# Kernel tuning notes

Measured on AMD Instinct MI355X. Metric: run time of the kernel, lower is better.

Reference implementation:

```python
import jax, jax.numpy as jnp
import numpy as np

N_NODES = 100000


def _gcn_conv(x, src, dst, dinv, W, b, n):
    # x: [n, din] -> [n, dout]; PyG GCNConv: transform, then normalized scatter-sum, then bias
    h = x @ W                                   # [n, dout]
    norm = dinv[src] * dinv[dst]                # [E'] symmetric normalization
    msg = h[src] * norm[:, None]                # gather + scale (irregular access)
    out = jax.ops.segment_sum(msg, dst, num_segments=n)
    return out + b


def _add_self_loops(edge_index, n):
    loop = jnp.arange(n, dtype=edge_index.dtype)
    src = jnp.concatenate([edge_index[0], loop])
    dst = jnp.concatenate([edge_index[1], loop])
    return src, dst


def setup_inputs() -> dict:
    key = jax.random.key(0)
    k1, k2, k3, k4 = jax.random.split(key, 4)
    n, e = N_NODES, 1000000
    din, dhid, dout = 512, 512, 128
    x = jax.random.normal(k1, (n, din), dtype=jnp.float32)
    edge_index = jax.random.randint(k2, (2, e), 0, n, dtype=jnp.int64)
    W1 = jax.random.normal(k3, (din, dhid), dtype=jnp.float32) * (1.0 / np.sqrt(din))
    b1 = jnp.zeros((dhid,), dtype=jnp.float32)
    W2 = jax.random.normal(k4, (dhid, dout), dtype=jnp.float32) * (1.0 / np.sqrt(dhid))
    b2 = jnp.zeros((dout,), dtype=jnp.float32)
    return {"x": x, "edge_index": edge_index, "original_size": n,
            "W1": W1, "b1": b1, "W2": W2, "b2": b2}


def reference(x, edge_index, original_size, W1, b1, W2, b2):
    n = x.shape[0]
    src, dst = _add_self_loops(edge_index, n)
    # degree over destination (with self-loops deg >= 1)
    deg = jnp.zeros((n,), dtype=x.dtype).at[dst].add(1.0)
    dinv = deg ** -0.5
    h = _gcn_conv(x, src, dst, dinv, W1, b1, n)
    out = _gcn_conv(h, src, dst, dinv, W2, b2, n)
    return out[:original_size]
```

## Files before the change

### kernel.cpp

```cpp
#include <hip/hip_runtime.h>
#include <hip/hip_bf16.h>


typedef __attribute__((ext_vector_type(8))) short short8;
typedef __attribute__((ext_vector_type(4))) float f32x4;

#define DIN 512
#define DOUT 128

__device__ inline short f2bs(float f) {
    __hip_bfloat16 h = __float2bfloat16(f);
    return __builtin_bit_cast(short, h);
}
__device__ inline float b2f(const void* p, long long idx) {
    return __bfloat162float(((const __hip_bfloat16*)p)[idx]);
}
__device__ inline int edge_at(const void* ei, int eflag, long long idx) {
    return eflag ? ((const int*)ei)[idx] : (int)((const long long*)ei)[idx];
}

__global__ void k_fdetect(const unsigned short* __restrict__ xr, int* __restrict__ fflag) {
    __shared__ int cnt;
    if (threadIdx.x == 0) cnt = 0;
    __syncthreads();
    int local = 0;
    for (int i = threadIdx.x; i < 8192; i += 256) {
        unsigned e = (xr[i] >> 7) & 0xFF;
        if (e == 0 || (e >= 0x70 && e <= 0x8E)) local++;
    }
    atomicAdd(&cnt, local);
    __syncthreads();
    if (threadIdx.x == 0) *fflag = (cnt >= 7373) ? 1 : 0;
}

__global__ void k_edetect(const int* __restrict__ ei_raw, int* __restrict__ eflag) {
    __shared__ int any;
    if (threadIdx.x == 0) any = 0;
    __syncthreads();
    for (int i = threadIdx.x; i < 4096; i += 256)
        if (ei_raw[2 * i + 1] != 0) any = 1;
    __syncthreads();
    if (threadIdx.x == 0) *eflag = any;
}

__global__ __launch_bounds__(256) void k_w12(const void* __restrict__ W1,
                                             const void* __restrict__ W2,
                                             const int* __restrict__ fflag,
                                             __hip_bfloat16* __restrict__ w12p) {
    int t = blockIdx.x * 256 + threadIdx.x;
    int d = t >> 7, j = t & 127;
    float acc = 0.f;
    if (*fflag) {
        for (int c = 0; c < 512; ++c)
            acc += b2f(W1, d * 512 + c) * b2f(W2, c * 128 + j);
    } else {
        const float* w1 = (const float*)W1;
        const float* w2 = (const float*)W2;
        for (int c = 0; c < 512; ++c)
            acc += w1[d * 512 + c] * w2[c * 128 + j];
    }
    int ks = d >> 5, r = d & 31;
    int quad = r >> 3, jj = r & 7;
    int nc = j >> 4, m16 = j & 15;
    w12p[(((size_t)(ks * 8 + nc) * 64) + quad * 16 + m16) * 8 + jj] = __float2bfloat16(acc);
}

__global__ void k_b12(const void* __restrict__ b1, const void* __restrict__ W2,
                      const int* __restrict__ fflag, float* __restrict__ b12) {
    int j = threadIdx.x;
    float acc = 0.f;
    if (*fflag) {
        for (int c = 0; c < 512; ++c)
            acc += b2f(b1, c) * b2f(W2, c * 128 + j);
    } else {
        const float* bb = (const float*)b1;
        const float* w2 = (const float*)W2;
        for (int c = 0; c < 512; ++c)
            acc += bb[c] * w2[c * 128 + j];
    }
    b12[j] = acc;
}

__global__ __launch_bounds__(256) void k_deg(const void* __restrict__ ei,
                                             const int* __restrict__ eflag, int E,
                                             int* __restrict__ degi) {
    int e = blockIdx.x * 256 + threadIdx.x;
    if (e >= E) return;
    atomicAdd(&degi[edge_at(ei, *eflag, (long long)E + e)], 1);
}

__global__ __launch_bounds__(256) void k_scan1(const int* __restrict__ degi,
                                               int* __restrict__ row_ptr,
                                               int* __restrict__ blocksum,
                                               float* __restrict__ dinv, int n) {
    __shared__ int sh[256];
    int t = threadIdx.x, g = blockIdx.x * 256 + t;
    int val = (g < n) ? degi[g] : 0;
    if (g < n) dinv[g] = rsqrtf((float)(val + 1));
    sh[t] = val;
    __syncthreads();
    for (int o = 1; o < 256; o <<= 1) {
        int v = (t >= o) ? sh[t - o] : 0;
        __syncthreads();
        if (t >= o) sh[t] += v;
        __syncthreads();
    }
    if (g < n) row_ptr[g] = sh[t] - val;
    if (t == 255) blocksum[blockIdx.x] = sh[255];
}

__global__ void k_scan2(int* __restrict__ blocksum, int nb) {
    __shared__ int sh[512];
    int t = threadIdx.x;
    int val = (t < nb) ? blocksum[t] : 0;
    sh[t] = val;
    __syncthreads();
    for (int o = 1; o < 512; o <<= 1) {
        int v = (t >= o) ? sh[t - o] : 0;
        __syncthreads();
        if (t >= o) sh[t] += v;
        __syncthreads();
    }
    if (t < nb) blocksum[t] = sh[t] - val;
}

__global__ __launch_bounds__(256) void k_scan3(int* __restrict__ row_ptr,
                                               int* __restrict__ cursor,
                                               const int* __restrict__ blocksum,
                                               int n, int E) {
    int g = blockIdx.x * 256 + threadIdx.x;
    if (g == 0) row_ptr[n] = E;
    if (g >= n) return;
    int v = row_ptr[g] + blocksum[blockIdx.x];
    row_ptr[g] = v;
    cursor[g] = v;
}

__global__ __launch_bounds__(256) void k_fill(const void* __restrict__ ei,
                                              const int* __restrict__ eflag, int E,
                                              const float* __restrict__ dinv,
                                              int* __restrict__ cursor,
                                              int2* __restrict__ csr) {
    int e = blockIdx.x * 256 + threadIdx.x;
    if (e >= E) return;
    int f = *eflag;
    int s = edge_at(ei, f, e);
    int d = edge_at(ei, f, (long long)E + e);
    int pos = atomicAdd(&cursor[d], 1);
    csr[pos] = make_int2(s, __float_as_int(dinv[s]));
}

__global__ __launch_bounds__(256) void k_gemm(const void* __restrict__ xv,
                                              const short* __restrict__ w12p,
                                              const int* __restrict__ fflag,
                                              float* __restrict__ M, int n) {
    int wave = (blockIdx.x * 256 + threadIdx.x) >> 6;
    int lane = threadIdx.x & 63;
    int row0 = wave * 16;
    if (row0 >= n) return;
    int quad = lane >> 4, m16 = lane & 15;
    const short8* Bp = (const short8*)w12p;

    f32x4 acc[8];
#pragma unroll
    for (int j = 0; j < 8; ++j) acc[j] = (f32x4){0.f, 0.f, 0.f, 0.f};

    int ra = row0 + m16;
    if (ra >= n) ra = n - 1;

    if (*fflag) {
        const short* xs = (const short*)xv;
#pragma unroll 4
        for (int ks = 0; ks < 16; ++ks) {
            int k0 = ks * 32 + quad * 8;
            short8 A0 = *(const short8*)(xs + (size_t)ra * 512 + k0);
#pragma unroll
            for (int nc = 0; nc < 8; ++nc) {
                short8 B = Bp[(ks * 8 + nc) * 64 + lane];
                acc[nc] = __builtin_amdgcn_mfma_f32_16x16x32_bf16(A0, B, acc[nc], 0, 0, 0);
            }
        }
    } else {
        const float* xf = (const float*)xv;
#pragma unroll 4
        for (int ks = 0; ks < 16; ++ks) {
            int k0 = ks * 32 + quad * 8;
            float4 u0 = *(const float4*)(xf + (size_t)ra * 512 + k0);
            float4 u1 = *(const float4*)(xf + (size_t)ra * 512 + k0 + 4);
            short8 A0;
            A0[0] = f2bs(u0.x); A0[1] = f2bs(u0.y); A0[2] = f2bs(u0.z); A0[3] = f2bs(u0.w);
            A0[4] = f2bs(u1.x); A0[5] = f2bs(u1.y); A0[6] = f2bs(u1.z); A0[7] = f2bs(u1.w);
#pragma unroll
            for (int nc = 0; nc < 8; ++nc) {
                short8 B = Bp[(ks * 8 + nc) * 64 + lane];
                acc[nc] = __builtin_amdgcn_mfma_f32_16x16x32_bf16(A0, B, acc[nc], 0, 0, 0);
            }
        }
    }
#pragma unroll
    for (int nc = 0; nc < 8; ++nc)
#pragma unroll
        for (int r = 0; r < 4; ++r) {
            int row = row0 + quad * 4 + r;
            if (row < n)
                M[(size_t)row * 128 + nc * 16 + m16] = acc[nc][r];
        }
}

template <bool FINAL>
__global__ __launch_bounds__(256) void k_gather(const int* __restrict__ row_ptr,
                                                const int2* __restrict__ csr,
                                                const float* __restrict__ dinv,
                                                const float* __restrict__ src_feat,
                                                float* __restrict__ dstf,
                                                const float* __restrict__ b12,
                                                const void* __restrict__ b2,
                                                const int* __restrict__ fflag,
                                                void* __restrict__ out, int n) {
    int d = blockIdx.x * 4 + (threadIdx.x >> 6);
    if (d >= n) return;
    int lane = threadIdx.x & 63;
    int half = lane >> 5, sl = lane & 31;
    int c = sl * 4;
    float di = dinv[d];
    float ax = 0.f, ay = 0.f, az = 0.f, aw = 0.f, wsum = 0.f;
    if (half == 0) {
        float4 s = *(const float4*)(src_feat + (size_t)d * 128 + c);
        ax = di * s.x; ay = di * s.y; az = di * s.z; aw = di * s.w;
    }
    int beg = row_ptr[d], end = row_ptr[d + 1];
    for (int e = beg + half; e < end; e += 2) {
        int2 rec = csr[e];
        float w = __int_as_float(rec.y);
        float4 v = *(const float4*)(src_feat + (size_t)rec.x * 128 + c);
        ax += w * v.x; ay += w * v.y; az += w * v.z; aw += w * v.w;
        wsum += w;
    }
    ax += __shfl_xor(ax, 32);
    ay += __shfl_xor(ay, 32);
    az += __shfl_xor(az, 32);
    aw += __shfl_xor(aw, 32);
    wsum += __shfl_xor(wsum, 32);
    if (half) return;
    ax *= di; ay *= di; az *= di; aw *= di;
    if (!FINAL) {
        *(float4*)(dstf + (size_t)d * 128 + c) = make_float4(ax, ay, az, aw);
    } else {
        float coef = di * (wsum + di);
        float o0 = ax + coef * b12[c];
        float o1 = ay + coef * b12[c + 1];
        float o2 = az + coef * b12[c + 2];
        float o3 = aw + coef * b12[c + 3];
        if (*fflag) {
            o0 += b2f(b2, c);     o1 += b2f(b2, c + 1);
            o2 += b2f(b2, c + 2); o3 += b2f(b2, c + 3);
            ushort4 u = make_ushort4((unsigned short)f2bs(o0), (unsigned short)f2bs(o1),
                                     (unsigned short)f2bs(o2), (unsigned short)f2bs(o3));
            *(ushort4*)((unsigned short*)out + (size_t)d * 128 + c) = u;
        } else {
            o0 += ((const float*)b2)[c];
            o1 += ((const float*)b2)[c + 1];
            o2 += ((const float*)b2)[c + 2];
            o3 += ((const float*)b2)[c + 3];
            *(float4*)((float*)out + (size_t)d * 128 + c) = make_float4(o0, o1, o2, o3);
        }
    }
}

__global__ __launch_bounds__(256) void k_sentinel(unsigned short* __restrict__ out, int total) {
    int t = blockIdx.x * 256 + threadIdx.x;
    if (t < total) out[t] = 0x4641;
}

extern "C" void kernel_launch(void* const* d_in, const int* in_sizes, int n_in,
                              void* d_out, int out_size, void* d_ws, size_t ws_size,
                              hipStream_t stream) {
    const int n = out_size / DOUT;

    const void *x = nullptr, *W1 = nullptr, *b1 = nullptr, *W2 = nullptr, *b2 = nullptr;
    const void* ei_raw = nullptr;
    int E = 0;
    const long long nx = (long long)n * DIN;
    for (int i = 0; i < n_in; ++i) {
        long long s = in_sizes[i];
        if      (s == nx && !x)                      x  = d_in[i];
        else if (s == (long long)DIN * DIN && !W1)   W1 = d_in[i];
        else if (s == (long long)DIN && !b1)         b1 = d_in[i];
        else if (s == (long long)DIN * DOUT && !W2)  W2 = d_in[i];
        else if (s == (long long)DOUT && !b2)        b2 = d_in[i];
        else if (s == 1) {  }
        else if (!ei_raw) { ei_raw = d_in[i]; E = (int)(s / 2); }
    }
    if (!x || !W1 || !b1 || !W2 || !b2 || !ei_raw) {
        x  = d_in[0];
        ei_raw = d_in[1];  E = in_sizes[1] / 2;
        W1 = d_in[3]; b1 = d_in[4]; W2 = d_in[5]; b2 = d_in[6];
    }

    const int nb_scan = (n + 255) / 256;

    char* ws = (char*)d_ws;
    size_t off = 0;
    auto alloc = [&](size_t bytes) { void* p = ws + off; off = (off + bytes + 255) & ~255ULL; return p; };
    int*   eflag    = (int*)alloc(4);
    int*   fflag    = (int*)alloc(4);
    int*   degi     = (int*)alloc((size_t)n * 4);
    float* dinv     = (float*)alloc((size_t)n * 4);
    float* b12      = (float*)alloc(DOUT * 4);
    __hip_bfloat16* w12p = (__hip_bfloat16*)alloc(DIN * DOUT * 2);
    int*   row_ptr  = (int*)alloc(((size_t)n + 1) * 4);
    int*   cursor   = (int*)alloc((size_t)n * 4);
    int*   blocksum = (int*)alloc(512 * 4);
    int2*  csr      = (int2*)alloc((size_t)E * 8);
    float* M        = (float*)alloc((size_t)n * DOUT * 4);
    float* B1       = (float*)alloc((size_t)n * DOUT * 4);

    if (ws_size < off) {
        k_sentinel<<<(out_size + 255) / 256, 256, 0, stream>>>((unsigned short*)d_out, out_size);
        return;
    }

    hipMemsetAsync(degi, 0, (size_t)n * 4, stream);

    k_fdetect<<<1, 256, 0, stream>>>((const unsigned short*)x, fflag);
    k_edetect<<<1, 256, 0, stream>>>((const int*)ei_raw, eflag);

    k_w12<<<(DIN * DOUT) / 256, 256, 0, stream>>>(W1, W2, fflag, w12p);
    k_b12<<<1, 128, 0, stream>>>(b1, W2, fflag, b12);

    k_deg<<<(E + 255) / 256, 256, 0, stream>>>(ei_raw, eflag, E, degi);
    k_scan1<<<nb_scan, 256, 0, stream>>>(degi, row_ptr, blocksum, dinv, n);
    k_scan2<<<1, 512, 0, stream>>>(blocksum, nb_scan);
    k_scan3<<<nb_scan, 256, 0, stream>>>(row_ptr, cursor, blocksum, n, E);
    k_fill<<<(E + 255) / 256, 256, 0, stream>>>(ei_raw, eflag, E, dinv, cursor, csr);

    int waves = (n + 15) / 16;
    k_gemm<<<(waves + 3) / 4, 256, 0, stream>>>(x, (const short*)w12p, fflag, M, n);

    int nb_g = (n + 3) / 4;
    k_gather<false><<<nb_g, 256, 0, stream>>>(row_ptr, csr, dinv, M, B1,
                                              nullptr, nullptr, fflag, nullptr, n);
    k_gather<true><<<nb_g, 256, 0, stream>>>(row_ptr, csr, dinv, B1, nullptr,
                                             b12, b2, fflag, d_out, n);
}
```

Before: 697.2 us.

## Vectorize W12 precompute, tile GEMM over 64 rows, batch gather rows per wave

```diff
diff --git a/kernel.cpp b/kernel.cpp
--- a/kernel.cpp
+++ b/kernel.cpp
@@ -14,6 +14,9 @@
 }
 __device__ inline float b2f(const void* p, long long idx) {
     return __bfloat162float(((const __hip_bfloat16*)p)[idx]);
+}
+__device__ inline float bsu(unsigned short v) {
+    return __bfloat162float(__builtin_bit_cast(__hip_bfloat16, v));
 }
 __device__ inline int edge_at(const void* ei, int eflag, long long idx) {
     return eflag ? ((const int*)ei)[idx] : (int)((const long long*)ei)[idx];
@@ -48,21 +51,44 @@
                                              const int* __restrict__ fflag,
                                              __hip_bfloat16* __restrict__ w12p) {
     int t = blockIdx.x * 256 + threadIdx.x;
-    int d = t >> 7, j = t & 127;
-    float acc = 0.f;
+    int d = t >> 5, j0 = (t & 31) * 4;
+    float4 acc = make_float4(0.f, 0.f, 0.f, 0.f);
     if (*fflag) {
-        for (int c = 0; c < 512; ++c)
-            acc += b2f(W1, d * 512 + c) * b2f(W2, c * 128 + j);
+        const short* w1s = (const short*)W1;
+        const unsigned short* w2u = (const unsigned short*)W2;
+        for (int c8 = 0; c8 < 512; c8 += 8) {
+            short8 av = *(const short8*)(w1s + (size_t)d * 512 + c8);
+#pragma unroll
+            for (int k = 0; k < 8; ++k) {
+                float a = bsu((unsigned short)av[k]);
+                ushort4 u = *(const ushort4*)(w2u + (size_t)(c8 + k) * 128 + j0);
+                acc.x += a * bsu(u.x); acc.y += a * bsu(u.y);
+                acc.z += a * bsu(u.z); acc.w += a * bsu(u.w);
+            }
+        }
     } else {
         const float* w1 = (const float*)W1;
         const float* w2 = (const float*)W2;
-        for (int c = 0; c < 512; ++c)
-            acc += w1[d * 512 + c] * w2[c * 128 + j];
+        for (int c4 = 0; c4 < 512; c4 += 4) {
+            float4 a  = *(const float4*)(w1 + (size_t)d * 512 + c4);
+            float4 r0 = *(const float4*)(w2 + (size_t)(c4 + 0) * 128 + j0);
+            float4 r1 = *(const float4*)(w2 + (size_t)(c4 + 1) * 128 + j0);
+            float4 r2 = *(const float4*)(w2 + (size_t)(c4 + 2) * 128 + j0);
+            float4 r3 = *(const float4*)(w2 + (size_t)(c4 + 3) * 128 + j0);
+            acc.x += a.x * r0.x + a.y * r1.x + a.z * r2.x + a.w * r3.x;
+            acc.y += a.x * r0.y + a.y * r1.y + a.z * r2.y + a.w * r3.y;
+            acc.z += a.x * r0.z + a.y * r1.z + a.z * r2.z + a.w * r3.z;
+            acc.w += a.x * r0.w + a.y * r1.w + a.z * r2.w + a.w * r3.w;
+        }
     }
     int ks = d >> 5, r = d & 31;
     int quad = r >> 3, jj = r & 7;
-    int nc = j >> 4, m16 = j & 15;
-    w12p[(((size_t)(ks * 8 + nc) * 64) + quad * 16 + m16) * 8 + jj] = __float2bfloat16(acc);
+    float av[4] = {acc.x, acc.y, acc.z, acc.w};
+#pragma unroll
+    for (int q = 0; q < 4; ++q) {
+        int j = j0 + q, nc = j >> 4, m16 = j & 15;
+        w12p[(((size_t)(ks * 8 + nc) * 64) + quad * 16 + m16) * 8 + jj] = __float2bfloat16(av[q]);
+    }
 }
 
 __global__ void k_b12(const void* __restrict__ b1, const void* __restrict__ W2,
@@ -150,119 +176,160 @@
     csr[pos] = make_int2(s, __float_as_int(dinv[s]));
 }
 
-__global__ __launch_bounds__(256) void k_gemm(const void* __restrict__ xv,
-                                              const short* __restrict__ w12p,
-                                              const int* __restrict__ fflag,
-                                              float* __restrict__ M, int n) {
-    int wave = (blockIdx.x * 256 + threadIdx.x) >> 6;
-    int lane = threadIdx.x & 63;
-    int row0 = wave * 16;
+__global__ __launch_bounds__(64, 1) void k_gemm(const void* __restrict__ xv,
+                                                const short* __restrict__ w12p,
+                                                const int* __restrict__ fflag,
+                                                float* __restrict__ M, int n) {
+    int lane = threadIdx.x;
+    int row0 = blockIdx.x * 64;
     if (row0 >= n) return;
     int quad = lane >> 4, m16 = lane & 15;
     const short8* Bp = (const short8*)w12p;
 
-    f32x4 acc[8];
-#pragma unroll
-    for (int j = 0; j < 8; ++j) acc[j] = (f32x4){0.f, 0.f, 0.f, 0.f};
-
-    int ra = row0 + m16;
-    if (ra >= n) ra = n - 1;
+    f32x4 acc[4][8];
+#pragma unroll
+    for (int g = 0; g < 4; ++g)
+#pragma unroll
+        for (int nc = 0; nc < 8; ++nc) acc[g][nc] = (f32x4){0.f, 0.f, 0.f, 0.f};
+
+    int ra[4];
+#pragma unroll
+    for (int g = 0; g < 4; ++g) {
+        int r = row0 + g * 16 + m16;
+        ra[g] = (r < n) ? r : (n - 1);
+    }
 
     if (*fflag) {
         const short* xs = (const short*)xv;
-#pragma unroll 4
         for (int ks = 0; ks < 16; ++ks) {
             int k0 = ks * 32 + quad * 8;
-            short8 A0 = *(const short8*)(xs + (size_t)ra * 512 + k0);
-#pragma unroll
-            for (int nc = 0; nc < 8; ++nc) {
-                short8 B = Bp[(ks * 8 + nc) * 64 + lane];
-                acc[nc] = __builtin_amdgcn_mfma_f32_16x16x32_bf16(A0, B, acc[nc], 0, 0, 0);
+            short8 B[8];
+#pragma unroll
+            for (int nc = 0; nc < 8; ++nc) B[nc] = Bp[(ks * 8 + nc) * 64 + lane];
+#pragma unroll
+            for (int g = 0; g < 4; ++g) {
+                short8 A = *(const short8*)(xs + (size_t)ra[g] * 512 + k0);
+#pragma unroll
+                for (int nc = 0; nc < 8; ++nc)
+                    acc[g][nc] = __builtin_amdgcn_mfma_f32_16x16x32_bf16(B[nc], A, acc[g][nc], 0, 0, 0);
             }
         }
     } else {
         const float* xf = (const float*)xv;
-#pragma unroll 4
         for (int ks = 0; ks < 16; ++ks) {
             int k0 = ks * 32 + quad * 8;
-            float4 u0 = *(const float4*)(xf + (size_t)ra * 512 + k0);
-            float4 u1 = *(const float4*)(xf + (size_t)ra * 512 + k0 + 4);
-            short8 A0;
-            A0[0] = f2bs(u0.x); A0[1] = f2bs(u0.y); A0[2] = f2bs(u0.z); A0[3] = f2bs(u0.w);
-            A0[4] = f2bs(u1.x); A0[5] = f2bs(u1.y); A0[6] = f2bs(u1.z); A0[7] = f2bs(u1.w);
-#pragma unroll
-            for (int nc = 0; nc < 8; ++nc) {
-                short8 B = Bp[(ks * 8 + nc) * 64 + lane];
-                acc[nc] = __builtin_amdgcn_mfma_f32_16x16x32_bf16(A0, B, acc[nc], 0, 0, 0);
+            short8 B[8];
+#pragma unroll
+            for (int nc = 0; nc < 8; ++nc) B[nc] = Bp[(ks * 8 + nc) * 64 + lane];
+#pragma unroll
+            for (int g = 0; g < 4; ++g) {
+                float4 u0 = *(const float4*)(xf + (size_t)ra[g] * 512 + k0);
+                float4 u1 = *(const float4*)(xf + (size_t)ra[g] * 512 + k0 + 4);
+                short8 A;
+                A[0] = f2bs(u0.x); A[1] = f2bs(u0.y); A[2] = f2bs(u0.z); A[3] = f2bs(u0.w);
+                A[4] = f2bs(u1.x); A[5] = f2bs(u1.y); A[6] = f2bs(u1.z); A[7] = f2bs(u1.w);
+#pragma unroll
+                for (int nc = 0; nc < 8; ++nc)
+                    acc[g][nc] = __builtin_amdgcn_mfma_f32_16x16x32_bf16(B[nc], A, acc[g][nc], 0, 0, 0);
             }
         }
     }
 #pragma unroll
-    for (int nc = 0; nc < 8; ++nc)
-#pragma unroll
-        for (int r = 0; r < 4; ++r) {
-            int row = row0 + quad * 4 + r;
-            if (row < n)
-                M[(size_t)row * 128 + nc * 16 + m16] = acc[nc][r];
-        }
-}
+    for (int g = 0; g < 4; ++g) {
+        int rowr = row0 + g * 16 + m16;
+        if (rowr < n) {
+#pragma unroll
+            for (int nc = 0; nc < 8; ++nc)
+                *(f32x4*)(M + (size_t)rowr * 128 + nc * 16 + quad * 4) = acc[g][nc];
+        }
+    }
+}
+
+#define GC 16
 
 template <bool FINAL>
 __global__ __launch_bounds__(256) void k_gather(const int* __restrict__ row_ptr,
                                                 const int2* __restrict__ csr,
-                                                const float* __restrict__ dinv,
                                                 const float* __restrict__ src_feat,
                                                 float* __restrict__ dstf,
                                                 const float* __restrict__ b12,
                                                 const void* __restrict__ b2,
                                                 const int* __restrict__ fflag,
-                                                void* __restrict__ out, int n) {
-    int d = blockIdx.x * 4 + (threadIdx.x >> 6);
-    if (d >= n) return;
+                                                void* __restrict__ out, int n, int E) {
+    int wave = (blockIdx.x * 256 + threadIdx.x) >> 6;
     int lane = threadIdx.x & 63;
     int half = lane >> 5, sl = lane & 31;
     int c = sl * 4;
-    float di = dinv[d];
-    float ax = 0.f, ay = 0.f, az = 0.f, aw = 0.f, wsum = 0.f;
-    if (half == 0) {
-        float4 s = *(const float4*)(src_feat + (size_t)d * 128 + c);
-        ax = di * s.x; ay = di * s.y; az = di * s.z; aw = di * s.w;
-    }
-    int beg = row_ptr[d], end = row_ptr[d + 1];
-    for (int e = beg + half; e < end; e += 2) {
-        int2 rec = csr[e];
-        float w = __int_as_float(rec.y);
-        float4 v = *(const float4*)(src_feat + (size_t)rec.x * 128 + c);
-        ax += w * v.x; ay += w * v.y; az += w * v.z; aw += w * v.w;
-        wsum += w;
-    }
-    ax += __shfl_xor(ax, 32);
-    ay += __shfl_xor(ay, 32);
-    az += __shfl_xor(az, 32);
-    aw += __shfl_xor(aw, 32);
-    wsum += __shfl_xor(wsum, 32);
-    if (half) return;
-    ax *= di; ay *= di; az *= di; aw *= di;
-    if (!FINAL) {
-        *(float4*)(dstf + (size_t)d * 128 + c) = make_float4(ax, ay, az, aw);
-    } else {
-        float coef = di * (wsum + di);
-        float o0 = ax + coef * b12[c];
-        float o1 = ay + coef * b12[c + 1];
-        float o2 = az + coef * b12[c + 2];
-        float o3 = aw + coef * b12[c + 3];
-        if (*fflag) {
-            o0 += b2f(b2, c);     o1 += b2f(b2, c + 1);
-            o2 += b2f(b2, c + 2); o3 += b2f(b2, c + 3);
-            ushort4 u = make_ushort4((unsigned short)f2bs(o0), (unsigned short)f2bs(o1),
-                                     (unsigned short)f2bs(o2), (unsigned short)f2bs(o3));
-            *(ushort4*)((unsigned short*)out + (size_t)d * 128 + c) = u;
+    int d0 = wave * GC;
+    if (d0 >= n) return;
+
+    int rpq = min(d0 + lane, n);
+    int rpv = row_ptr[rpq];
+
+    float4 bv = make_float4(0.f, 0.f, 0.f, 0.f);
+    float4 b2v = make_float4(0.f, 0.f, 0.f, 0.f);
+    int ff = 0;
+    if (FINAL) {
+        ff = *fflag;
+        bv = *(const float4*)(b12 + c);
+        if (ff) {
+            ushort4 u = *(const ushort4*)((const unsigned short*)b2 + c);
+            b2v = make_float4(bsu(u.x), bsu(u.y), bsu(u.z), bsu(u.w));
         } else {
-            o0 += ((const float*)b2)[c];
-            o1 += ((const float*)b2)[c + 1];
-            o2 += ((const float*)b2)[c + 2];
-            o3 += ((const float*)b2)[c + 3];
-            *(float4*)((float*)out + (size_t)d * 128 + c) = make_float4(o0, o1, o2, o3);
+            b2v = *(const float4*)((const float*)b2 + c);
+        }
+    }
+
+    for (int i = 0; i < GC; ++i) {
+        int d = d0 + i;
+        if (d >= n) break;
+        int beg = __shfl(rpv, i);
+        int end = __shfl(rpv, i + 1);
+        int deg = end - beg;
+        float di = rsqrtf((float)(deg + 1));
+
+        float ax = 0.f, ay = 0.f, az = 0.f, aw = 0.f, wsum = 0.f;
+        if (half == 0) {
+            float4 s = *(const float4*)(src_feat + (size_t)d * 128 + c);
+            ax = di * s.x; ay = di * s.y; az = di * s.z; aw = di * s.w;
+        }
+        for (int ch = 0; ch < deg; ch += 64) {
+            int idx = beg + ch + lane;
+            if (idx >= E) idx = E - 1;
+            if (idx < 0) idx = 0;
+            int2 rec = csr[idx];
+            int lim = deg - ch; if (lim > 64) lim = 64;
+            for (int t = half; t < lim; t += 2) {
+                int srcn = __shfl(rec.x, t);
+                float w = __int_as_float(__shfl(rec.y, t));
+                float4 v = *(const float4*)(src_feat + (size_t)srcn * 128 + c);
+                ax += w * v.x; ay += w * v.y; az += w * v.z; aw += w * v.w;
+                wsum += w;
+            }
+        }
+        ax += __shfl_xor(ax, 32);
+        ay += __shfl_xor(ay, 32);
+        az += __shfl_xor(az, 32);
+        aw += __shfl_xor(aw, 32);
+        wsum += __shfl_xor(wsum, 32);
+        if (half == 0) {
+            ax *= di; ay *= di; az *= di; aw *= di;
+            if (!FINAL) {
+                *(float4*)(dstf + (size_t)d * 128 + c) = make_float4(ax, ay, az, aw);
+            } else {
+                float coef = di * (wsum + di);
+                float o0 = ax + coef * bv.x + b2v.x;
+                float o1 = ay + coef * bv.y + b2v.y;
+                float o2 = az + coef * bv.z + b2v.z;
+                float o3 = aw + coef * bv.w + b2v.w;
+                if (ff) {
+                    ushort4 u = make_ushort4((unsigned short)f2bs(o0), (unsigned short)f2bs(o1),
+                                             (unsigned short)f2bs(o2), (unsigned short)f2bs(o3));
+                    *(ushort4*)((unsigned short*)out + (size_t)d * 128 + c) = u;
+                } else {
+                    *(float4*)((float*)out + (size_t)d * 128 + c) = make_float4(o0, o1, o2, o3);
+                }
+            }
         }
     }
 }
@@ -296,6 +363,7 @@
         ei_raw = d_in[1];  E = in_sizes[1] / 2;
         W1 = d_in[3]; b1 = d_in[4]; W2 = d_in[5]; b2 = d_in[6];
     }
+    if (E < 1) E = 1;
 
     const int nb_scan = (n + 255) / 256;
 
@@ -325,7 +393,7 @@
     k_fdetect<<<1, 256, 0, stream>>>((const unsigned short*)x, fflag);
     k_edetect<<<1, 256, 0, stream>>>((const int*)ei_raw, eflag);
 
-    k_w12<<<(DIN * DOUT) / 256, 256, 0, stream>>>(W1, W2, fflag, w12p);
+    k_w12<<<(DIN * 32) / 256, 256, 0, stream>>>(W1, W2, fflag, w12p);
     k_b12<<<1, 128, 0, stream>>>(b1, W2, fflag, b12);
 
     k_deg<<<(E + 255) / 256, 256, 0, stream>>>(ei_raw, eflag, E, degi);
@@ -334,12 +402,12 @@
     k_scan3<<<nb_scan, 256, 0, stream>>>(row_ptr, cursor, blocksum, n, E);
     k_fill<<<(E + 255) / 256, 256, 0, stream>>>(ei_raw, eflag, E, dinv, cursor, csr);
 
-    int waves = (n + 15) / 16;
-    k_gemm<<<(waves + 3) / 4, 256, 0, stream>>>(x, (const short*)w12p, fflag, M, n);
-
-    int nb_g = (n + 3) / 4;
-    k_gather<false><<<nb_g, 256, 0, stream>>>(row_ptr, csr, dinv, M, B1,
-                                              nullptr, nullptr, fflag, nullptr, n);
-    k_gather<true><<<nb_g, 256, 0, stream>>>(row_ptr, csr, dinv, B1, nullptr,
-                                             b12, b2, fflag, d_out, n);
-}
+    k_gemm<<<(n + 63) / 64, 64, 0, stream>>>(x, (const short*)w12p, fflag, M, n);
+
+    int gwaves = (n + GC - 1) / GC;
+    int gb = (gwaves + 3) / 4;
+    k_gather<false><<<gb, 256, 0, stream>>>(row_ptr, csr, M, B1,
+                                            nullptr, nullptr, fflag, nullptr, n, E);
+    k_gather<true><<<gb, 256, 0, stream>>>(row_ptr, csr, B1, nullptr,
+                                           b12, b2, fflag, d_out, n, E);
+}
```

Result: faster. 659.4 us (-5.4%).
